# Optimization experiments

Measured on AMD Instinct MI355X. Metric: run time of the kernel, lower is better.

Reference implementation:

```python
import jax, jax.numpy as jnp
import numpy as np

B, T, D = 64, 512, 384
MAX_LEN = 4096


def setup_inputs() -> dict:
    key = jax.random.key(0)
    kx, kd = jax.random.split(key)
    x = jax.random.normal(kx, (B, T, D), dtype=jnp.float32)
    duration = jax.random.randint(kd, (B, T), 0, 8, dtype=jnp.int32)
    return {"x": x, "duration": duration, "max_len": MAX_LEN}


def reference(x, duration, max_len):
    # x: [B, T, D], duration: [B, T] int, max_len: python int
    # Cumsum trick replaces the per-row repeat_interleave + cat + pad:
    # token t of row b occupies output rows [csum[t-1], csum[t]).
    csum = jnp.cumsum(duration, axis=1)                       # [B, T]
    mel_len = csum[:, -1]                                     # [B]
    pos = jnp.arange(max_len, dtype=csum.dtype)               # [M]
    # For each output position m, index of source token: first t with csum[t] > m
    idx = jax.vmap(lambda c: jnp.searchsorted(c, pos, side="right"))(csum)  # [B, M]
    idx = jnp.minimum(idx, x.shape[1] - 1)
    out = jnp.take_along_axis(x, idx[:, :, None], axis=1)     # [B, M, D]
    mask = (pos[None, :] < mel_len[:, None])[:, :, None]      # [B, M, 1]
    out = jnp.where(mask, out, jnp.zeros((), dtype=out.dtype))
    return out, mel_len
```

## Files before the change

### kernel.cpp

```cpp
#include <hip/hip_runtime.h>


#define T_DIM 512
#define D_DIM 384
#define D4    (D_DIM / 4)
#define ROWS  32
#define BLOCK 512
#define ITER  ((ROWS * D4) / BLOCK)

typedef float vfloat4 __attribute__((ext_vector_type(4)));

__global__ __launch_bounds__(BLOCK) void lr_scan_idx_kernel(
    const int* __restrict__ duration,
    int*       __restrict__ idx,
    float*     __restrict__ mel_out,
    int ML)
{
    __shared__ int s_csum[T_DIM];
    const int b   = blockIdx.x;
    const int tid = threadIdx.x;

    s_csum[tid] = duration[b * T_DIM + tid];
    __syncthreads();

    for (int off = 1; off < T_DIM; off <<= 1) {
        int v = (tid >= off) ? s_csum[tid - off] : 0;
        __syncthreads();
        s_csum[tid] += v;
        __syncthreads();
    }
    const int mel = s_csum[T_DIM - 1];
    if (tid == 0) mel_out[b] = (float)mel;

    int* __restrict__ idx_b = idx + b * ML;

    const int start = (tid == 0) ? 0 : s_csum[tid - 1];
    const int end   = s_csum[tid];
    for (int p = start; p < end; ++p) idx_b[p] = tid;

    for (int p = mel + tid; p < ML; p += BLOCK) idx_b[p] = -1;
}

__global__ __launch_bounds__(BLOCK) void lr_copy_kernel(
    const float* __restrict__ x,
    const int*   __restrict__ idx,
    float*       __restrict__ out,
    int B, int ML)
{
    __shared__ int s_idx[ROWS];

    const int b     = blockIdx.x % B;
    const int chunk = blockIdx.x / B;
    const int row0  = chunk * ROWS;
    const int tid   = threadIdx.x;

    if (tid < ROWS) s_idx[tid] = idx[b * ML + row0 + tid];
    __syncthreads();

    const vfloat4* __restrict__ x4   = (const vfloat4*)x;
    vfloat4*       __restrict__ out4 = (vfloat4*)out;

    const long long out_base = ((long long)b * ML + row0) * D4;
    const long long x_base   = (long long)b * T_DIM * D4;

    #pragma unroll
    for (int i = 0; i < ITER; ++i) {
        const int flat = tid + i * BLOCK;
        const int r = flat / D4;
        const int j = flat - r * D4;
        const int t = s_idx[r];
        vfloat4 v = (vfloat4)(0.f, 0.f, 0.f, 0.f);
        if (t >= 0) v = x4[x_base + (long long)t * D4 + j];
        out4[out_base + flat] = v;
    }
}

extern "C" void kernel_launch(void* const* d_in, const int* in_sizes, int n_in,
                              void* d_out, int out_size, void* d_ws, size_t ws_size,
                              hipStream_t stream) {
    const float* x   = (const float*)d_in[0];
    const int*   dur = (const int*)d_in[1];
    float*       out = (float*)d_out;
    int*         idx = (int*)d_ws;

    const int B  = in_sizes[1] / T_DIM;
    const int ML = (out_size - B) / (B * D_DIM);

    float* mel_out = out + (long long)B * ML * D_DIM;

    hipLaunchKernelGGL(lr_scan_idx_kernel, dim3(B), dim3(BLOCK), 0, stream,
                       dur, idx, mel_out, ML);

    const int grid = B * (ML / ROWS);
    hipLaunchKernelGGL(lr_copy_kernel, dim3(grid), dim3(BLOCK), 0, stream,
                       x, idx, out, B, ML);
}
```

Before: 434.8 us.

## Fuse scan and copy into one kernel with per-block binary search

Merges the cumsum/index-building kernel into the copy kernel. Each block recomputes the row's prefix sum with wave shuffles plus a cross-wave combine, then binary-searches the source token for each of its output rows. This removes a launch, the idx workspace round-trip and the serial per-token idx writes. The cost is a redundant scan in every block, and doubling ROWS halves the block count to offset that.

```diff
diff --git a/kernel.cpp b/kernel.cpp
--- a/kernel.cpp
+++ b/kernel.cpp
@@ -4,62 +4,67 @@
 #define T_DIM 512
 #define D_DIM 384
 #define D4    (D_DIM / 4)
-#define ROWS  32
+#define ROWS  64
 #define BLOCK 512
 #define ITER  ((ROWS * D4) / BLOCK)
+#define NWAVE (BLOCK / 64)
 
 typedef float vfloat4 __attribute__((ext_vector_type(4)));
 
-__global__ __launch_bounds__(BLOCK) void lr_scan_idx_kernel(
-    const int* __restrict__ duration,
-    int*       __restrict__ idx,
-    float*     __restrict__ mel_out,
-    int ML)
-{
-    __shared__ int s_csum[T_DIM];
-    const int b   = blockIdx.x;
-    const int tid = threadIdx.x;
-
-    s_csum[tid] = duration[b * T_DIM + tid];
-    __syncthreads();
-
-    for (int off = 1; off < T_DIM; off <<= 1) {
-        int v = (tid >= off) ? s_csum[tid - off] : 0;
-        __syncthreads();
-        s_csum[tid] += v;
-        __syncthreads();
-    }
-    const int mel = s_csum[T_DIM - 1];
-    if (tid == 0) mel_out[b] = (float)mel;
-
-    int* __restrict__ idx_b = idx + b * ML;
-
-    const int start = (tid == 0) ? 0 : s_csum[tid - 1];
-    const int end   = s_csum[tid];
-    for (int p = start; p < end; ++p) idx_b[p] = tid;
-
-    for (int p = mel + tid; p < ML; p += BLOCK) idx_b[p] = -1;
-}
-
-__global__ __launch_bounds__(BLOCK) void lr_copy_kernel(
+__global__ __launch_bounds__(BLOCK) void lr_fused_kernel(
     const float* __restrict__ x,
-    const int*   __restrict__ idx,
+    const int*   __restrict__ duration,
     float*       __restrict__ out,
     int B, int ML)
 {
+    __shared__ int s_csum[T_DIM];
+    __shared__ int s_wsum[NWAVE];
     __shared__ int s_idx[ROWS];
 
     const int b     = blockIdx.x % B;
     const int chunk = blockIdx.x / B;
     const int row0  = chunk * ROWS;
     const int tid   = threadIdx.x;
+    const int lane  = tid & 63;
+    const int wid   = tid >> 6;
 
-    if (tid < ROWS) s_idx[tid] = idx[b * ML + row0 + tid];
+    int v = duration[b * T_DIM + tid];
+    #pragma unroll
+    for (int off = 1; off < 64; off <<= 1) {
+        int u = __shfl_up(v, off);
+        if (lane >= off) v += u;
+    }
+    if (lane == 63) s_wsum[wid] = v;
+    __syncthreads();
+    int wprefix = 0;
+    #pragma unroll
+    for (int w = 0; w < NWAVE - 1; ++w)
+        if (w < wid) wprefix += s_wsum[w];
+    s_csum[tid] = wprefix + v;
+    __syncthreads();
+
+    const int mel = s_csum[T_DIM - 1];
+    if (chunk == 0 && tid == 0)
+        out[(long long)B * ML * D_DIM + b] = (float)mel;
+
+    if (tid < ROWS) {
+        const int p = row0 + tid;
+        int t = -1;
+        if (p < mel) {
+            int lo = 0, hi = T_DIM;
+            #pragma unroll
+            for (int step = 0; step < 9; ++step) {
+                const int mid = (lo + hi) >> 1;
+                if (s_csum[mid] <= p) lo = mid + 1; else hi = mid;
+            }
+            t = lo;
+        }
+        s_idx[tid] = t;
+    }
     __syncthreads();
 
     const vfloat4* __restrict__ x4   = (const vfloat4*)x;
     vfloat4*       __restrict__ out4 = (vfloat4*)out;
-
     const long long out_base = ((long long)b * ML + row0) * D4;
     const long long x_base   = (long long)b * T_DIM * D4;
 
@@ -69,9 +74,9 @@
         const int r = flat / D4;
         const int j = flat - r * D4;
         const int t = s_idx[r];
-        vfloat4 v = (vfloat4)(0.f, 0.f, 0.f, 0.f);
-        if (t >= 0) v = x4[x_base + (long long)t * D4 + j];
-        out4[out_base + flat] = v;
+        vfloat4 vv = (vfloat4)(0.f, 0.f, 0.f, 0.f);
+        if (t >= 0) vv = x4[x_base + (long long)t * D4 + j];
+        out4[out_base + flat] = vv;
     }
 }
 
@@ -81,17 +86,12 @@
     const float* x   = (const float*)d_in[0];
     const int*   dur = (const int*)d_in[1];
     float*       out = (float*)d_out;
-    int*         idx = (int*)d_ws;
+    (void)d_ws; (void)ws_size;
 
     const int B  = in_sizes[1] / T_DIM;
     const int ML = (out_size - B) / (B * D_DIM);
 
-    float* mel_out = out + (long long)B * ML * D_DIM;
-
-    hipLaunchKernelGGL(lr_scan_idx_kernel, dim3(B), dim3(BLOCK), 0, stream,
-                       dur, idx, mel_out, ML);
-
     const int grid = B * (ML / ROWS);
-    hipLaunchKernelGGL(lr_copy_kernel, dim3(grid), dim3(BLOCK), 0, stream,
-                       x, idx, out, B, ML);
+    hipLaunchKernelGGL(lr_fused_kernel, dim3(grid), dim3(BLOCK), 0, stream,
+                       x, dur, out, B, ML);
 }
```

Measured after the change: 431.5 us. About the same (-0.8%).
